# Kernel optimization log

Measured on AMD Instinct MI355X. Metric: run time of the kernel, lower is better.

The kernel has to match this reference:

```python
import jax, jax.numpy as jnp
import numpy as np

B = 4096   # batch
NC = 1     # input channels
K1 = 30    # layer-1 channels
K2 = 80    # layer-2 channels
P = 3      # pooling window (p_x = p_y = 3)
H = 28     # input spatial size (forced: 28 -> conv8 -> 21 -> pool3 -> 7 -> conv4 -> 4)


def _conv(x, w):
    # torch Conv2d (valid, stride 1, no bias): x NCHW, w OIHW
    return jax.lax.conv_general_dilated(x, w, (1, 1), 'VALID',
                                        dimension_numbers=('NCHW', 'OIHW', 'NCHW'))


def _conv_t(x, w):
    # torch ConvTranspose2d (stride 1, no pad, no bias). w: [in, out, kh, kw].
    # Equivalent to full cross-correlation with spatially-flipped, channel-swapped kernel.
    k = w.shape[2]
    wf = jnp.flip(w, (2, 3)).transpose(1, 0, 2, 3)  # -> OIHW
    return jax.lax.conv_general_dilated(x, wf, (1, 1), [(k - 1, k - 1), (k - 1, k - 1)],
                                        dimension_numbers=('NCHW', 'OIHW', 'NCHW'))


def setup_inputs() -> dict:
    key = jax.random.key(0)
    ks = jax.random.split(key, 12)
    sc = 0.05
    f32 = jnp.float32
    return {
        'x':        jax.random.normal(ks[0], (B, NC, H, H), f32),
        'enc1_w':   jax.random.normal(ks[1], (K1, NC, 8, 8), f32) * sc,   # Conv2d OIHW
        'pool_w1':  jax.random.normal(ks[2], (9, 9), f32) * sc,           # Linear [out,in], no bias
        'pool_w2':  jax.random.normal(ks[3], (9, 9), f32) * sc,
        'enc2_w':   jax.random.normal(ks[4], (K2, K1, 4, 4), f32) * sc,
        'h_w':      jax.random.normal(ks[5], (K2, 16, 16), f32) * sc,     # stacked Linear(16,16) [out,in]
        'h_b':      jnp.zeros((K2, 16), f32),
        'mean_w':   jax.random.normal(ks[6], (K2, 16, 16), f32) * sc,
        'mean_b':   jnp.zeros((K2, 16), f32),
        'logvar_w': jax.random.normal(ks[7], (K2, 16, 16), f32) * sc,
        'logvar_b': jnp.zeros((K2, 16), f32),
        'dec2_w':   jax.random.normal(ks[8], (K2, K1, 4, 4), f32) * sc,   # ConvTranspose [in,out,kh,kw]
        'dec1_w':   jax.random.normal(ks[9], (K1, NC, 8, 8), f32) * sc,
        'alpha':    jnp.asarray(0.5, f32),
    }


def reference(x, enc1_w, pool_w1, pool_w2, enc2_w, h_w, h_b,
              mean_w, mean_b, logvar_w, logvar_b, dec2_w, dec1_w, alpha):
    k_pool, k_unpool, k_code, k_noise = jax.random.split(jax.random.key(42), 4)

    # --- encoder conv 1 ---
    c1 = _conv(x, enc1_w)                               # [B, K1, 21, 21]
    b, c, hp, wp = c1.shape
    n, m = hp // P, wp // P                             # 7, 7

    # --- stochastic pooling (vectorized over B, K1, n, m tiles) ---
    tiles = c1.reshape(b, c, n, P, m, P).transpose(0, 1, 2, 4, 3, 5)
    tiles = tiles.reshape(b, c, n, m, P * P)            # [B,K1,7,7,9]
    h1 = jnp.tanh(jnp.einsum('bcnmt,ot->bcnmo', tiles, pool_w1))
    eta = jax.nn.softmax(jnp.einsum('bcnmt,ot->bcnmo', h1, pool_w2), axis=-1)
    zeta = jax.random.categorical(k_pool, jnp.log(eta))  # [B,K1,7,7]
    pooled = jnp.take_along_axis(tiles, zeta[..., None], axis=-1)[..., 0]  # [B,K1,7,7]

    # --- encoder conv 2 + per-channel code MLPs ---
    c2 = _conv(pooled, enc2_w)                          # [B, K2, 4, 4]
    flat = c2.reshape(b, K2, 16)                        # [B, K2, 16]
    h = jnp.tanh(jnp.einsum('bki,koi->bko', flat, h_w) + h_b)
    mean = jnp.einsum('bki,koi->bko', h, mean_w) + mean_b      # [B,K2,16]
    log_var = jnp.einsum('bki,koi->bko', h, logvar_w) + logvar_b

    # --- reparameterized sample per channel ---
    std = jnp.exp(0.5 * log_var)
    s = (mean + std * jax.random.normal(k_code, mean.shape, mean.dtype)).reshape(c2.shape)

    # --- decoder ---
    s2 = _conv_t(s, dec2_w)                             # [B, K1, 7, 7]

    # stochastic unpooling: fresh multinomial draw from the same etas, scatter into tile
    zeta2 = jax.random.categorical(k_unpool, jnp.log(eta))      # [B,K1,7,7]
    tiles_u = jax.nn.one_hot(zeta2, P * P, dtype=s2.dtype) * s2[..., None]  # [B,K1,7,7,9]
    s1 = tiles_u.reshape(b, c, n, m, P, P).transpose(0, 1, 2, 4, 3, 5).reshape(b, c, n * P, m * P)
    s1 = _conv_t(s1, dec1_w)                            # [B, NC, 28, 28]

    # --- add_noise: std = (1/alpha) * eye(H, W), zero std off-diagonal ---
    noise_std = (1.0 / alpha) * jnp.eye(s1.shape[-2], s1.shape[-1], dtype=s1.dtype)
    x_rec = s1 + noise_std * jax.random.normal(k_noise, s1.shape, s1.dtype)

    return x_rec, mean, log_var, eta
```

## Files before the change

### kernel.cpp

```cpp
#include <hip/hip_runtime.h>
#include <cstdint>


#define OFF_MEAN 3211264
#define OFF_LV   8454144
#define OFF_ETA  13697024

constexpr uint64_t ctf(uint32_t k0, uint32_t k1, uint32_t x0, uint32_t x1) {
  uint32_t ks0 = k0, ks1 = k1, ks2 = k0 ^ k1 ^ 0x1BD11BDAu;
  const int rotA[4] = {13, 15, 26, 6};
  const int rotB[4] = {17, 29, 16, 24};
  x0 += ks0; x1 += ks1;
  for (int g = 0; g < 5; ++g) {
    for (int i = 0; i < 4; ++i) {
      int r = (g & 1) ? rotB[i] : rotA[i];
      x0 += x1;
      x1 = (uint32_t)((x1 << r) | (x1 >> (32 - r)));
      x1 ^= x0;
    }
    uint32_t ka = (g + 1) % 3 == 0 ? ks0 : ((g + 1) % 3 == 1 ? ks1 : ks2);
    uint32_t kb = (g + 2) % 3 == 0 ? ks0 : ((g + 2) % 3 == 1 ? ks1 : ks2);
    x0 += ka;
    x1 += kb + (uint32_t)(g + 1);
  }
  return ((uint64_t)x0 << 32) | (uint64_t)x1;
}

constexpr uint64_t KP_ = ctf(0u, 42u, 0u, 0u);
constexpr uint64_t KU_ = ctf(0u, 42u, 0u, 1u);
constexpr uint64_t KC_ = ctf(0u, 42u, 0u, 2u);
constexpr uint64_t KN_ = ctf(0u, 42u, 0u, 3u);
constexpr uint32_t KPOOL0 = (uint32_t)(KP_ >> 32), KPOOL1 = (uint32_t)KP_;
constexpr uint32_t KUNP0  = (uint32_t)(KU_ >> 32), KUNP1  = (uint32_t)KU_;
constexpr uint32_t KCODE0 = (uint32_t)(KC_ >> 32), KCODE1 = (uint32_t)KC_;
constexpr uint32_t KNOIS0 = (uint32_t)(KN_ >> 32), KNOIS1 = (uint32_t)KN_;

__device__ __forceinline__ uint2 tf_dev(uint32_t k0, uint32_t k1, uint32_t x0, uint32_t x1) {
  uint32_t ks2 = k0 ^ k1 ^ 0x1BD11BDAu;
  x0 += k0; x1 += k1;
#define TFR(r) { x0 += x1; x1 = (x1 << (r)) | (x1 >> (32 - (r))); x1 ^= x0; }
  TFR(13) TFR(15) TFR(26) TFR(6)
  x0 += k1;  x1 += ks2 + 1u;
  TFR(17) TFR(29) TFR(16) TFR(24)
  x0 += ks2; x1 += k0 + 2u;
  TFR(13) TFR(15) TFR(26) TFR(6)
  x0 += k0;  x1 += k1 + 3u;
  TFR(17) TFR(29) TFR(16) TFR(24)
  x0 += k1;  x1 += ks2 + 4u;
  TFR(13) TFR(15) TFR(26) TFR(6)
  x0 += ks2; x1 += k0 + 5u;
#undef TFR
  return make_uint2(x0, x1);
}

__device__ __forceinline__ uint32_t rbits32(uint32_t k0, uint32_t k1, uint32_t idx) {
  uint2 r = tf_dev(k0, k1, 0u, idx);
  return r.x ^ r.y;
}

__device__ __forceinline__ float u01_from_bits(uint32_t bits) {
  return __uint_as_float((bits >> 9) | 0x3F800000u) - 1.0f;
}

__device__ __forceinline__ float gumbel_draw(uint32_t k0, uint32_t k1, uint32_t idx) {
  float u01 = u01_from_bits(rbits32(k0, k1, idx));
  float u = fmaxf(__fadd_rn(u01, 1.17549435e-38f), 1.17549435e-38f);
  return -logf(-logf(u));
}

__device__ __forceinline__ float erfinv_xla(float x) {
  float t = __fmul_rn(x, x);
  float w = -log1pf(-t);
  float p;
  if (w < 5.0f) {
    w = __fadd_rn(w, -2.5f);
    p = 2.81022636e-08f;
    p = __fadd_rn(__fmul_rn(p, w), 3.43273939e-07f);
    p = __fadd_rn(__fmul_rn(p, w), -3.5233877e-06f);
    p = __fadd_rn(__fmul_rn(p, w), -4.39150654e-06f);
    p = __fadd_rn(__fmul_rn(p, w), 0.00021858087f);
    p = __fadd_rn(__fmul_rn(p, w), -0.00125372503f);
    p = __fadd_rn(__fmul_rn(p, w), -0.00417768164f);
    p = __fadd_rn(__fmul_rn(p, w), 0.246640727f);
    p = __fadd_rn(__fmul_rn(p, w), 1.50140941f);
  } else {
    w = __fadd_rn(sqrtf(w), -3.0f);
    p = -0.000200214257f;
    p = __fadd_rn(__fmul_rn(p, w), 0.000100950558f);
    p = __fadd_rn(__fmul_rn(p, w), 0.00134934322f);
    p = __fadd_rn(__fmul_rn(p, w), -0.00367342844f);
    p = __fadd_rn(__fmul_rn(p, w), 0.00573950773f);
    p = __fadd_rn(__fmul_rn(p, w), -0.0076224613f);
    p = __fadd_rn(__fmul_rn(p, w), 0.00943887047f);
    p = __fadd_rn(__fmul_rn(p, w), 1.00167406f);
    p = __fadd_rn(__fmul_rn(p, w), 2.83297682f);
  }
  return __fmul_rn(p, x);
}

__device__ __forceinline__ float normal_draw(uint32_t k0, uint32_t k1, uint32_t idx) {
  float u01 = u01_from_bits(rbits32(k0, k1, idx));
  float u = fmaxf(__fadd_rn(__fmul_rn(u01, 2.0f), -0.99999994f), -0.99999994f);
  return __fmul_rn(1.41421356237309515f, erfinv_xla(u));
}

__device__ __forceinline__ float tanh_xla(float x) {
  float ax = fabsf(x);
  float xc = fmaxf(fminf(x, 7.90531110763549805f), -7.90531110763549805f);
  float x2 = __fmul_rn(xc, xc);
  float p = __fmaf_rn(x2, -2.76076847742355e-16f, 2.00018790482477e-13f);
  p = __fmaf_rn(x2, p, -8.60467152213735e-11f);
  p = __fmaf_rn(x2, p, 5.12229709037114e-08f);
  p = __fmaf_rn(x2, p, 1.48572235717979e-05f);
  p = __fmaf_rn(x2, p, 6.37261928875436e-04f);
  p = __fmaf_rn(x2, p, 4.89352455891786e-03f);
  p = __fmul_rn(xc, p);
  float q = __fmaf_rn(x2, 1.19825839466702e-06f, 1.18534705686654e-04f);
  q = __fmaf_rn(x2, q, 2.26843463243900e-03f);
  q = __fmaf_rn(x2, q, 4.89352518554385e-03f);
  return (ax < 0.0004f) ? x : __fdiv_rn(p, q);
}

__global__ __launch_bounds__(256) void k_enc(
    const float* __restrict__ x, const float* __restrict__ enc1_w,
    const float* __restrict__ pw1, const float* __restrict__ pw2,
    const float* __restrict__ enc2_w, const float* __restrict__ h_w,
    const float* __restrict__ h_b, const float* __restrict__ mean_w,
    const float* __restrict__ mean_b, const float* __restrict__ lv_w,
    const float* __restrict__ lv_b,
    float* __restrict__ o_mean, float* __restrict__ o_lv, float* __restrict__ o_eta,
    float* __restrict__ ws_s, unsigned char* __restrict__ ws_z) {
  __shared__ float lds[2866];
  __shared__ float pooled[1470];
  const int b = blockIdx.x, tid = threadIdx.x;

  float* xs  = lds;
  float* w1s = lds + 784;
  float* pp1 = lds + 2704;
  float* pp2 = lds + 2785;
  for (int i = tid; i < 784; i += 256) xs[i] = x[(size_t)b * 784 + i];
  for (int i = tid; i < 1920; i += 256) w1s[i] = enc1_w[i];
  if (tid < 81) { pp1[tid] = pw1[tid]; pp2[tid] = pw2[tid]; }
  __syncthreads();

  for (int g = tid; g < 1470; g += 256) {
    const int c = g / 49, cell = g - c * 49;
    const int n = cell / 7, m = cell - n * 7;
    const int yb = n * 3, xb = m * 3;
    const float* wc = &w1s[c * 64];

    float R[3][10];
#pragma unroll
    for (int rr = 0; rr < 3; ++rr)
#pragma unroll
      for (int i = 0; i < 10; ++i) R[rr][i] = xs[(yb + rr) * 28 + xb + i];

    float tile[9];
#pragma unroll
    for (int i = 0; i < 9; ++i) tile[i] = 0.f;

#pragma unroll
    for (int dy = 0; dy < 8; ++dy) {
      float4 wa = *(const float4*)&wc[dy * 8];
      float4 wb = *(const float4*)&wc[dy * 8 + 4];
      float w8[8] = {wa.x, wa.y, wa.z, wa.w, wb.x, wb.y, wb.z, wb.w};
#pragma unroll
      for (int dx = 0; dx < 8; ++dx) {
        float w = w8[dx];
#pragma unroll
        for (int p = 0; p < 3; ++p)
#pragma unroll
          for (int q = 0; q < 3; ++q)
            tile[p * 3 + q] = __fmaf_rn(R[(dy + p) % 3][dx + q], w, tile[p * 3 + q]);
      }
      if (dy < 7) {
#pragma unroll
        for (int i = 0; i < 10; ++i) R[dy % 3][i] = xs[(yb + dy + 3) * 28 + xb + i];
      }
    }

    float h1v[9];
#pragma unroll
    for (int o = 0; o < 9; ++o) {
      float a = 0.f;
#pragma unroll
      for (int t = 0; t < 9; ++t) a += tile[t] * pp1[o * 9 + t];
      h1v[o] = tanh_xla(a);
    }
    float lg[9], mx = -3.4e38f;
#pragma unroll
    for (int o = 0; o < 9; ++o) {
      float a = 0.f;
#pragma unroll
      for (int t = 0; t < 9; ++t) a += h1v[t] * pp2[o * 9 + t];
      lg[o] = a;
      mx = fmaxf(mx, a);
    }
    float ev[9], ssum = 0.f;
#pragma unroll
    for (int o = 0; o < 9; ++o) { ev[o] = expf(__fadd_rn(lg[o], -mx)); ssum += ev[o]; }
    float leta[9];
    size_t ebase = ((size_t)(b * 30 + c) * 49 + cell) * 9;
#pragma unroll
    for (int o = 0; o < 9; ++o) {
      float e = __fdiv_rn(ev[o], ssum);
      o_eta[ebase + o] = e;
      leta[o] = logf(e);
    }
    uint32_t fb = (uint32_t)ebase;
    float best1 = -3.4e38f, best2 = -3.4e38f, pooledv = 0.f;
    int z2 = 0;
#pragma unroll
    for (int t = 0; t < 9; ++t) {
      float v1 = __fadd_rn(leta[t], gumbel_draw(KPOOL0, KPOOL1, fb + t));
      bool t1 = v1 > best1; best1 = t1 ? v1 : best1; pooledv = t1 ? tile[t] : pooledv;
      float v2 = __fadd_rn(leta[t], gumbel_draw(KUNP0, KUNP1, fb + t));
      bool t2 = v2 > best2; best2 = t2 ? v2 : best2; z2 = t2 ? t : z2;
    }
    pooled[g] = pooledv;
    ws_z[(size_t)b * 1470 + g] = (unsigned char)z2;
  }
  __syncthreads();

  float* c2s = lds;
  float* hs  = lds + 1280;
  const int k2l = tid >> 4, pos = tid & 15;
  const int uy = pos >> 2, ux = pos & 3;
  {
    float acc[5] = {0.f, 0.f, 0.f, 0.f, 0.f};
    for (int c = 0; c < 30; ++c) {
      float pr[16];
#pragma unroll
      for (int dy = 0; dy < 4; ++dy)
#pragma unroll
        for (int dx = 0; dx < 4; ++dx)
          pr[dy * 4 + dx] = pooled[c * 49 + (uy + dy) * 7 + ux + dx];
#pragma unroll
      for (int j = 0; j < 5; ++j) {
        const float4* wr = (const float4*)&enc2_w[(size_t)((j * 16 + k2l) * 30 + c) * 16];
        float4 w0 = wr[0], w1 = wr[1], w2 = wr[2], w3 = wr[3];
        float a = acc[j];
        a = __fmaf_rn(pr[0],  w0.x, a);  a = __fmaf_rn(pr[1],  w0.y, a);
        a = __fmaf_rn(pr[2],  w0.z, a);  a = __fmaf_rn(pr[3],  w0.w, a);
        a = __fmaf_rn(pr[4],  w1.x, a);  a = __fmaf_rn(pr[5],  w1.y, a);
        a = __fmaf_rn(pr[6],  w1.z, a);  a = __fmaf_rn(pr[7],  w1.w, a);
        a = __fmaf_rn(pr[8],  w2.x, a);  a = __fmaf_rn(pr[9],  w2.y, a);
        a = __fmaf_rn(pr[10], w2.z, a);  a = __fmaf_rn(pr[11], w2.w, a);
        a = __fmaf_rn(pr[12], w3.x, a);  a = __fmaf_rn(pr[13], w3.y, a);
        a = __fmaf_rn(pr[14], w3.z, a);  a = __fmaf_rn(pr[15], w3.w, a);
        acc[j] = a;
      }
    }
#pragma unroll
    for (int j = 0; j < 5; ++j) c2s[(j * 16 + k2l) * 16 + pos] = acc[j];
  }
  __syncthreads();

#pragma unroll
  for (int j = 0; j < 5; ++j) {
    int it = tid + j * 256;
    int k2 = it >> 4;
    const float4* wr4 = (const float4*)&h_w[(size_t)it * 16];
    float4 a0 = wr4[0], a1 = wr4[1], a2 = wr4[2], a3 = wr4[3];
    float wv16[16] = {a0.x, a0.y, a0.z, a0.w, a1.x, a1.y, a1.z, a1.w,
                      a2.x, a2.y, a2.z, a2.w, a3.x, a3.y, a3.z, a3.w};
    float d = 0.f;
#pragma unroll
    for (int i = 0; i < 16; ++i) d += c2s[k2 * 16 + i] * wv16[i];
    hs[it] = tanh_xla(__fadd_rn(d, h_b[it]));
  }
  __syncthreads();

#pragma unroll
  for (int j = 0; j < 5; ++j) {
    int it = tid + j * 256;
    int k2 = it >> 4;
    const float4* wm4 = (const float4*)&mean_w[(size_t)it * 16];
    const float4* wl4 = (const float4*)&lv_w[(size_t)it * 16];
    float4 m0 = wm4[0], m1 = wm4[1], m2 = wm4[2], m3 = wm4[3];
    float4 l0 = wl4[0], l1 = wl4[1], l2 = wl4[2], l3 = wl4[3];
    float wm16[16] = {m0.x, m0.y, m0.z, m0.w, m1.x, m1.y, m1.z, m1.w,
                      m2.x, m2.y, m2.z, m2.w, m3.x, m3.y, m3.z, m3.w};
    float wl16[16] = {l0.x, l0.y, l0.z, l0.w, l1.x, l1.y, l1.z, l1.w,
                      l2.x, l2.y, l2.z, l2.w, l3.x, l3.y, l3.z, l3.w};
    float dm = 0.f, dl = 0.f;
#pragma unroll
    for (int i = 0; i < 16; ++i) {
      float hv = hs[k2 * 16 + i];
      dm += hv * wm16[i];
      dl += hv * wl16[i];
    }
    float mean = __fadd_rn(dm, mean_b[it]);
    float lv = __fadd_rn(dl, lv_b[it]);
    size_t gi = (size_t)b * 1280 + it;
    o_mean[gi] = mean;
    o_lv[gi] = lv;
    float stdv = expf(__fmul_rn(0.5f, lv));
    float z = normal_draw(KCODE0, KCODE1, (uint32_t)(b * 1280 + it));
    ws_s[gi] = __fadd_rn(mean, __fmul_rn(stdv, z));
  }
}

__global__ __launch_bounds__(256) void k_expand(const float* __restrict__ dec2_w,
                                                float* __restrict__ Wexp) {
  int idx = blockIdx.x * 256 + threadIdx.x;
  int k = idx / 1472, t = idx - k * 1472;
  int k2 = k >> 4, iy = (k >> 2) & 3, ix = k & 3;
  int c = t / 49, cell = t - c * 49;
  int u = cell / 7, v = cell - u * 7;
  int du = u - iy, dv = v - ix;
  float val = 0.f;
  if (t < 1470 && (unsigned)du < 4u && (unsigned)dv < 4u)
    val = dec2_w[((k2 * 30 + c) << 4) + (du << 2) + dv];
  Wexp[idx] = val;
}

__global__ __launch_bounds__(256) void k_gemm(const float* __restrict__ A,
                                              const float* __restrict__ Bm,
                                              float* __restrict__ C) {
  __shared__ float As[16][68];
  __shared__ float Bs[16][128];
  const int tid = threadIdx.x;
  const int n0 = blockIdx.x * 128;
  const int m0 = blockIdx.y * 64;
  const int tx = tid & 15, ty = tid >> 4;

  float acc[4][8];
#pragma unroll
  for (int i = 0; i < 4; ++i)
#pragma unroll
    for (int j = 0; j < 8; ++j) acc[i][j] = 0.f;

  const int a_r = tid >> 2, a_c = (tid & 3) << 2;
  const int b_k = tid >> 4, b_c = (tid & 15) << 3;
  const int bcol = n0 + b_c;
  const int bcol_c = (bcol > 1464) ? 1464 : bcol;

  const float* pa = &A[(size_t)(m0 + a_r) * 1280 + a_c];
  const float* pb = &Bm[(size_t)b_k * 1472 + bcol_c];

  float4 av = *(const float4*)pa;
  float4 bv0 = *(const float4*)pb;
  float4 bv1 = *(const float4*)(pb + 4);

  for (int k0 = 0; k0 < 1280; k0 += 16) {
    __syncthreads();
    As[a_c + 0][a_r] = av.x;  As[a_c + 1][a_r] = av.y;
    As[a_c + 2][a_r] = av.z;  As[a_c + 3][a_r] = av.w;
    *(float4*)&Bs[b_k][b_c] = bv0;
    *(float4*)&Bs[b_k][b_c + 4] = bv1;
    __syncthreads();

    if (k0 + 16 < 1280) {
      av = *(const float4*)(pa + k0 + 16);
      bv0 = *(const float4*)(pb + (size_t)(k0 + 16) * 1472);
      bv1 = *(const float4*)(pb + (size_t)(k0 + 16) * 1472 + 4);
    }

#pragma unroll
    for (int kk = 0; kk < 16; ++kk) {
      float4 a4 = *(const float4*)&As[kk][ty * 4];
      float4 b4a = *(const float4*)&Bs[kk][tx * 8];
      float4 b4b = *(const float4*)&Bs[kk][tx * 8 + 4];
      float am[4] = {a4.x, a4.y, a4.z, a4.w};
      float bn[8] = {b4a.x, b4a.y, b4a.z, b4a.w, b4b.x, b4b.y, b4b.z, b4b.w};
#pragma unroll
      for (int i = 0; i < 4; ++i)
#pragma unroll
        for (int j = 0; j < 8; ++j) acc[i][j] = __fmaf_rn(am[i], bn[j], acc[i][j]);
    }
  }

  if (n0 + tx * 8 < 1472) {
#pragma unroll
    for (int i = 0; i < 4; ++i) {
      size_t row = (size_t)(m0 + ty * 4 + i);
      float4 o0 = make_float4(acc[i][0], acc[i][1], acc[i][2], acc[i][3]);
      float4 o1 = make_float4(acc[i][4], acc[i][5], acc[i][6], acc[i][7]);
      *(float4*)&C[row * 1472 + n0 + tx * 8] = o0;
      *(float4*)&C[row * 1472 + n0 + tx * 8 + 4] = o1;
    }
  }
}

__global__ __launch_bounds__(256) void k_unpool(
    const float* __restrict__ S2, const unsigned char* __restrict__ ws_z,
    const float* __restrict__ dec1_w, const float* __restrict__ alpha,
    float* __restrict__ o_xrec) {
  __shared__ float w1s[1920];
  __shared__ float2 tv[2][1470];
  const int b0 = blockIdx.x * 2, tid = threadIdx.x;

  for (int i = tid; i < 1920; i += 256) w1s[i] = dec1_w[i];
  for (int t = tid; t < 2940; t += 256) {
    int bb = t >= 1470;
    int tt = t - bb * 1470;
    int c = tt / 49, cell = tt - c * 49;
    int n = cell / 7, m = cell - n * 7;
    int b = b0 + bb;
    int z = ws_z[(size_t)b * 1470 + tt];
    int p = z / 3, q = z - p * 3;
    float val = S2[(size_t)b * 1472 + tt];
    tv[bb][tt] = make_float2(val, __uint_as_float((uint32_t)((n * 3 + p) | ((m * 3 + q) << 8))));
  }
  __syncthreads();

  float inva = __fdiv_rn(1.0f, alpha[0]);
  for (int pix = tid; pix < 1568; pix += 256) {
    int bb = pix >= 784;
    int p2 = pix - bb * 784;
    int b = b0 + bb;
    int y = p2 / 28, x = p2 - y * 28;
    int nlo = (y >= 9) ? ((y - 9 + 2) / 3) : 0;
    int nhi = min(6, y / 3);
    int mlo = (x >= 9) ? ((x - 9 + 2) / 3) : 0;
    int mhi = min(6, x / 3);

    float acc = 0.f;
    const float2* tvb = tv[bb];
    for (int c = 0; c < 30; ++c) {
      const float2* tvc = &tvb[c * 49];
      const float* wc = &w1s[c * 64];
#pragma unroll
      for (int dn = 0; dn < 4; ++dn) {
        int n = nlo + dn;
        bool nok = n <= nhi;
        int nn = nok ? n : nhi;
#pragma unroll
        for (int dm = 0; dm < 4; ++dm) {
          int m = mlo + dm;
          bool ok = nok && (m <= mhi);
          int mm = (m <= mhi) ? m : mhi;
          float2 tvv = tvc[nn * 7 + mm];
          uint32_t pp = __float_as_uint(tvv.y);
          int dy = y - (int)(pp & 0xffu);
          int dx = x - (int)(pp >> 8);
          ok = ok && ((unsigned)dy < 8u) && ((unsigned)dx < 8u);
          float wvv = wc[((dy & 7) << 3) + (dx & 7)];
          acc = __fmaf_rn(ok ? tvv.x : 0.f, wvv, acc);
        }
      }
    }
    if (y == x) {
      float zn = normal_draw(KNOIS0, KNOIS1, (uint32_t)(b * 784 + p2));
      acc = __fadd_rn(acc, __fmul_rn(inva, zn));
    }
    o_xrec[(size_t)b * 784 + p2] = acc;
  }
}

extern "C" void kernel_launch(void* const* d_in, const int* in_sizes, int n_in,
                              void* d_out, int out_size, void* d_ws, size_t ws_size,
                              hipStream_t stream) {
  const float* x      = (const float*)d_in[0];
  const float* enc1_w = (const float*)d_in[1];
  const float* pw1    = (const float*)d_in[2];
  const float* pw2    = (const float*)d_in[3];
  const float* enc2_w = (const float*)d_in[4];
  const float* h_w    = (const float*)d_in[5];
  const float* h_b    = (const float*)d_in[6];
  const float* mean_w = (const float*)d_in[7];
  const float* mean_b = (const float*)d_in[8];
  const float* lv_w   = (const float*)d_in[9];
  const float* lv_b   = (const float*)d_in[10];
  const float* dec2_w = (const float*)d_in[11];
  const float* dec1_w = (const float*)d_in[12];
  const float* alpha  = (const float*)d_in[13];

  float* out = (float*)d_out;
  float* o_xrec = out;
  float* o_mean = out + OFF_MEAN;
  float* o_lv   = out + OFF_LV;
  float* o_eta  = out + OFF_ETA;

  char* wsb = (char*)d_ws;
  float* ws_s = (float*)wsb;
  unsigned char* ws_z = (unsigned char*)(wsb + 20971520);
  float* Wexp = (float*)(wsb + 26992640);
  float* S2   = (float*)(wsb + 34529280);

  k_expand<<<dim3(7360), dim3(256), 0, stream>>>(dec2_w, Wexp);
  k_enc<<<dim3(4096), dim3(256), 0, stream>>>(
      x, enc1_w, pw1, pw2, enc2_w, h_w, h_b, mean_w, mean_b, lv_w, lv_b,
      o_mean, o_lv, o_eta, ws_s, ws_z);
  k_gemm<<<dim3(12, 64), dim3(256), 0, stream>>>(ws_s, Wexp, S2);
  k_unpool<<<dim3(2048), dim3(256), 0, stream>>>(S2, ws_z, dec1_w, alpha, o_xrec);
}
```

Before: 1.646 ms.

## Rewrite unpool transposed conv as row-parallel scatter with LDS atomics

The final transposed convolution is changed from a gather form, where each pixel loops over the 4x4 candidate cells of all 30 channels, to a scatter form. In the new form each lane owns one output row and atomically adds the 8-wide weighted contribution of each sampled cell into a shared-memory accumulator. This skips the predicated-off gather work, since only the one chosen position in each 3x3 tile is non-zero. The block shrinks to 64 threads, which lowers the parallelism per block. LDS float atomics add contention and serialization, and the lanes with rows 28-31 do no work.

```diff
diff --git a/kernel.cpp b/kernel.cpp
--- a/kernel.cpp
+++ b/kernel.cpp
@@ -383,16 +383,19 @@
   }
 }
 
-__global__ __launch_bounds__(256) void k_unpool(
+__global__ __launch_bounds__(64) void k_unpool(
     const float* __restrict__ S2, const unsigned char* __restrict__ ws_z,
     const float* __restrict__ dec1_w, const float* __restrict__ alpha,
     float* __restrict__ o_xrec) {
   __shared__ float w1s[1920];
-  __shared__ float2 tv[2][1470];
-  const int b0 = blockIdx.x * 2, tid = threadIdx.x;
-
-  for (int i = tid; i < 1920; i += 256) w1s[i] = dec1_w[i];
-  for (int t = tid; t < 2940; t += 256) {
+  __shared__ float2 tv[2][1472];
+  __shared__ float xacc[2][816];
+  const int b0 = blockIdx.x * 2;
+  const int lane = threadIdx.x;
+
+  for (int i = lane; i < 1920; i += 64) w1s[i] = dec1_w[i];
+  for (int i = lane; i < 1632; i += 64) (&xacc[0][0])[i] = 0.f;
+  for (int t = lane; t < 2940; t += 64) {
     int bb = t >= 1470;
     int tt = t - bb * 1470;
     int c = tt / 49, cell = tt - c * 49;
@@ -405,47 +408,50 @@
   }
   __syncthreads();
 
+  const int bb = lane >> 5;
+  const int row = lane & 31;
+  const bool rowok = row < 28;
+  float* xrow = &xacc[bb][row * 28];
+  const float2* tvb = tv[bb];
+
+  for (int c = 0; c < 30; ++c) {
+    const float* wc = &w1s[c * 64];
+    const float2* tvc = &tvb[c * 49];
+    for (int cell = 0; cell < 49; ++cell) {
+      float2 tvv = tvc[cell];
+      uint32_t pp = __float_as_uint(tvv.y);
+      int dy = row - (int)(pp & 0xffu);
+      if (rowok & ((unsigned)dy < 8u)) {
+        int px = (int)(pp >> 8);
+        float4 wa = *(const float4*)&wc[dy * 8];
+        float4 wb = *(const float4*)&wc[dy * 8 + 4];
+        float v = tvv.x;
+        float* xr = &xrow[px];
+        atomicAdd(&xr[0], v * wa.x);
+        atomicAdd(&xr[1], v * wa.y);
+        atomicAdd(&xr[2], v * wa.z);
+        atomicAdd(&xr[3], v * wa.w);
+        atomicAdd(&xr[4], v * wb.x);
+        atomicAdd(&xr[5], v * wb.y);
+        atomicAdd(&xr[6], v * wb.z);
+        atomicAdd(&xr[7], v * wb.w);
+      }
+    }
+  }
+  __syncthreads();
+
   float inva = __fdiv_rn(1.0f, alpha[0]);
-  for (int pix = tid; pix < 1568; pix += 256) {
-    int bb = pix >= 784;
-    int p2 = pix - bb * 784;
-    int b = b0 + bb;
-    int y = p2 / 28, x = p2 - y * 28;
-    int nlo = (y >= 9) ? ((y - 9 + 2) / 3) : 0;
-    int nhi = min(6, y / 3);
-    int mlo = (x >= 9) ? ((x - 9 + 2) / 3) : 0;
-    int mhi = min(6, x / 3);
-
-    float acc = 0.f;
-    const float2* tvb = tv[bb];
-    for (int c = 0; c < 30; ++c) {
-      const float2* tvc = &tvb[c * 49];
-      const float* wc = &w1s[c * 64];
-#pragma unroll
-      for (int dn = 0; dn < 4; ++dn) {
-        int n = nlo + dn;
-        bool nok = n <= nhi;
-        int nn = nok ? n : nhi;
-#pragma unroll
-        for (int dm = 0; dm < 4; ++dm) {
-          int m = mlo + dm;
-          bool ok = nok && (m <= mhi);
-          int mm = (m <= mhi) ? m : mhi;
-          float2 tvv = tvc[nn * 7 + mm];
-          uint32_t pp = __float_as_uint(tvv.y);
-          int dy = y - (int)(pp & 0xffu);
-          int dx = x - (int)(pp >> 8);
-          ok = ok && ((unsigned)dy < 8u) && ((unsigned)dx < 8u);
-          float wvv = wc[((dy & 7) << 3) + (dx & 7)];
-          acc = __fmaf_rn(ok ? tvv.x : 0.f, wvv, acc);
-        }
-      }
-    }
-    if (y == x) {
+  for (int pix = lane; pix < 1568; pix += 64) {
+    int b2 = pix >= 784;
+    int p2 = pix - b2 * 784;
+    int b = b0 + b2;
+    int y = p2 / 28, xx = p2 - y * 28;
+    float a = xacc[b2][p2];
+    if (y == xx) {
       float zn = normal_draw(KNOIS0, KNOIS1, (uint32_t)(b * 784 + p2));
-      acc = __fadd_rn(acc, __fmul_rn(inva, zn));
-    }
-    o_xrec[(size_t)b * 784 + p2] = acc;
+      a = __fadd_rn(a, __fmul_rn(inva, zn));
+    }
+    o_xrec[(size_t)b * 784 + p2] = a;
   }
 }
 
@@ -484,5 +490,5 @@
       x, enc1_w, pw1, pw2, enc2_w, h_w, h_b, mean_w, mean_b, lv_w, lv_b,
       o_mean, o_lv, o_eta, ws_s, ws_z);
   k_gemm<<<dim3(12, 64), dim3(256), 0, stream>>>(ws_s, Wexp, S2);
-  k_unpool<<<dim3(2048), dim3(256), 0, stream>>>(S2, ws_z, dec1_w, alpha, o_xrec);
-}
+  k_unpool<<<dim3(2048), dim3(64), 0, stream>>>(S2, ws_z, dec1_w, alpha, o_xrec);
+}
```

Result: slower. 3.320 ms (+101.7%).
